# Kernel optimization log

Measured on AMD Instinct MI355X. Metric: run time of the kernel, lower is better.

The kernel has to match this reference:

```python
import jax, jax.numpy as jnp
import numpy as np

B, L, D_MODEL, N_HEADS = 2, 2048, 1024, 16
RANK = max(N_HEADS, int(D_MODEL * 0.25))            # 256
RANK_PER_HEAD = RANK // N_HEADS                      # 16
HEAD_DIM = D_MODEL // N_HEADS                        # 64


def _rope_cos_sin(L, head_dim, dtype=jnp.float32):
    half = head_dim // 2
    theta = 1.0 / (10000.0 ** (jnp.arange(half, dtype=dtype) / half))
    angles = jnp.arange(L, dtype=dtype)[:, None] * theta[None, :]   # [L, half]
    return jnp.cos(angles), jnp.sin(angles)


def _apply_rope(x, cos, sin):
    # x: [B, L, H, D]; pairs (even, odd) rotated by per-position angle.
    B, L, H, D = x.shape
    xp = x.reshape(B, L, H, D // 2, 2)
    x0, x1 = xp[..., 0], xp[..., 1]
    c = cos[None, :, None, :]
    s = sin[None, :, None, :]
    r0 = x0 * c - x1 * s
    r1 = x0 * s + x1 * c
    return jnp.stack([r0, r1], axis=-1).reshape(B, L, H, D)


def setup_inputs() -> dict:
    key = jax.random.key(0)
    ks = jax.random.split(key, 7)
    x = jax.random.normal(ks[0], (B, L, D_MODEL), dtype=jnp.float32)
    mask = jax.random.randint(ks[1], (B, L), 0, 2, dtype=jnp.int32)
    scale = 0.02
    Wq = jax.random.normal(ks[2], (RANK, D_MODEL), dtype=jnp.float32) * scale
    Wk = jax.random.normal(ks[3], (RANK, D_MODEL), dtype=jnp.float32) * scale
    Wv = jax.random.normal(ks[4], (RANK, D_MODEL), dtype=jnp.float32) * scale
    xav_u = float(np.sqrt(6.0 / (HEAD_DIM + RANK_PER_HEAD)))
    U = jax.random.uniform(ks[5], (N_HEADS, HEAD_DIM, RANK_PER_HEAD), dtype=jnp.float32, minval=-xav_u, maxval=xav_u)
    V = jax.random.uniform(ks[6], (N_HEADS, RANK_PER_HEAD, HEAD_DIM), dtype=jnp.float32, minval=-xav_u, maxval=xav_u)
    return {"x": x, "Wq": Wq, "Wk": Wk, "Wv": Wv, "U": U, "V": V, "mask": mask}


def reference(x, Wq, Wk, Wv, U, V, mask):
    Bq, Lq, _ = x.shape
    H, HD, RH = U.shape
    q_low = (x @ Wq.T).reshape(Bq, Lq, H, RH)
    k_low = (x @ Wk.T).reshape(Bq, Lq, H, RH)
    v_low = (x @ Wv.T).reshape(Bq, Lq, H, RH)
    # up-project q/k to head_dim via shared U
    q = jnp.einsum('hdr,blhr->blhd', U, q_low)
    k = jnp.einsum('hdr,blhr->blhd', U, k_low)
    cos, sin = _rope_cos_sin(Lq, HD, x.dtype)
    q = _apply_rope(q, cos, sin)
    k = _apply_rope(k, cos, sin)
    attn = jnp.einsum('blhd,bmhd->bhlm', q, k) / jnp.sqrt(jnp.asarray(HD, x.dtype))
    key_mask = mask.astype(bool)[:, None, None, :]           # [B,1,1,M]
    attn = jnp.where(key_mask, attn, jnp.asarray(-jnp.inf, attn.dtype))
    attn = jax.nn.softmax(attn, axis=-1)
    out = jnp.einsum('bhlm,bmhr->blhr', attn, v_low)
    out = jnp.einsum('blhr,hrd->blhd', out, V)
    return out.reshape(Bq, Lq, H * HD)
```

## Files before the change

kernel.cpp:

```cpp
#include <hip/hip_runtime.h>
#include <hip/hip_bf16.h>

typedef unsigned short u16;
typedef unsigned int u32;
typedef __bf16 bf16x8 __attribute__((ext_vector_type(8)));
typedef float f32x4 __attribute__((ext_vector_type(4)));

#define NB 2
#define NL 2048
#define NDM 1024
#define NH 16
#define NHD 64
#define NRH 16
#define NCOL 2304

#define QSCL 0.18033688011112042f

#define AS1(p) ((const __attribute__((address_space(1))) void*)(p))
#define AS3(p) ((__attribute__((address_space(3))) void*)(p))

__device__ __forceinline__ u16 f2bf(float f) {
  u32 u = __builtin_bit_cast(u32, f);
  u32 r = (u + 0x7fffu + ((u >> 16) & 1u)) >> 16;
  return (u16)r;
}

__global__ void k_prep_weff(const float* __restrict__ Wq, const float* __restrict__ Wk,
                            const float* __restrict__ Wv, const float* __restrict__ U,
                            u16* __restrict__ Wall) {
  int idx = blockIdx.x * 256 + threadIdx.x;
  int col = idx & 1023;
  int row = idx >> 10;
  float acc;
  if (row < 2048) {
    const float* W = (row < 1024) ? Wq : Wk;
    int rr = row & 1023;
    int h = rr >> 6, d = rr & 63;
    const float* Uh = U + (h * NHD + d) * NRH;
    const float* Wr = W + (size_t)(h * NRH) * NDM + col;
    acc = 0.f;
#pragma unroll
    for (int r = 0; r < 16; ++r) acc += Uh[r] * Wr[(size_t)r * NDM];
  } else {
    acc = Wv[(size_t)(row - 2048) * NDM + col];
  }
  Wall[idx] = f2bf(acc);
}

__global__ void k_cast_x(const float* __restrict__ x, u16* __restrict__ xb) {
  int i = blockIdx.x * 256 + threadIdx.x;
  float2 v = *(const float2*)(x + (size_t)i * 2);
  ushort2 o;
  o.x = f2bf(v.x);
  o.y = f2bf(v.y);
  *(ushort2*)(xb + (size_t)i * 2) = o;
}

__global__ void k_cstab(float2* __restrict__ cstab) {
  int i = blockIdx.x * 256 + threadIdx.x;
  if (i >= NL * 32) return;
  int l = i >> 5, j = i & 31;
  float theta = 1.0f / powf(10000.0f, (float)j * (1.0f / 32.0f));
  float ang = (float)l * theta;
  cstab[i] = float2{cosf(ang), sinf(ang)};
}

__global__ void k_fbias(const int* __restrict__ mask, float* __restrict__ fb) {
  int i = blockIdx.x * 256 + threadIdx.x;
  fb[i] = mask[i] ? 0.f : -1e30f;
}

__global__ __launch_bounds__(256) void k_gemm(const u16* __restrict__ A,
                                              const u16* __restrict__ Bm,
                                              const float2* __restrict__ cstab,
                                              u16* __restrict__ qt,
                                              u16* __restrict__ ktb,
                                              u16* __restrict__ vT) {
  __shared__ char lds[32768];
  const int tid = threadIdx.x;
  const int wave = tid >> 6, lane = tid & 63;
  const int bm = blockIdx.x, bn = blockIdx.y;
  const int wr = wave >> 1, wc = wave & 1;
  const char* Ag = (const char*)(A + (size_t)bm * 128 * NDM);
  const char* Bg = (const char*)(Bm + (size_t)bn * 128 * NDM);
  f32x4 acc[4][4] = {};
  for (int kt = 0; kt < 16; ++kt) {
    __syncthreads();
#pragma unroll
    for (int i = 0; i < 4; ++i) {
      int off = wave * 4096 + i * 1024 + lane * 16;
      int src = off ^ ((off >> 3) & 0x70);
      int ga = (src >> 7) * 2048 + kt * 128 + (src & 127);
      __builtin_amdgcn_global_load_lds(AS1(Ag + ga), AS3(lds + wave * 4096 + i * 1024), 16, 0, 0);
      __builtin_amdgcn_global_load_lds(AS1(Bg + ga), AS3(lds + 16384 + wave * 4096 + i * 1024), 16, 0, 0);
    }
    __syncthreads();
#pragma unroll
    for (int kk = 0; kk < 2; ++kk) {
      bf16x8 af[4], bfr[4];
#pragma unroll
      for (int m = 0; m < 4; ++m) {
        int row = wr * 64 + m * 16 + (lane & 15);
        int byte = row * 128 + kk * 64 + ((lane >> 4) << 4);
        af[m] = *(const bf16x8*)(lds + (byte ^ ((row & 7) << 4)));
      }
#pragma unroll
      for (int n = 0; n < 4; ++n) {
        int row = wc * 64 + n * 16 + (lane & 15);
        int byte = row * 128 + kk * 64 + ((lane >> 4) << 4);
        bfr[n] = *(const bf16x8*)(lds + 16384 + (byte ^ ((row & 7) << 4)));
      }
#pragma unroll
      for (int m = 0; m < 4; ++m)
#pragma unroll
        for (int n = 0; n < 4; ++n)
          acc[m][n] = __builtin_amdgcn_mfma_f32_16x16x32_bf16(af[m], bfr[n], acc[m][n], 0, 0, 0);
    }
  }

  const int r0 = bm * 128 + wr * 64;
  const int b = r0 >> 11;
  if (bn < 16) {
    const bool isq = (bn < 8);
    u16* dst = isq ? qt : ktb;
    const float qs = isq ? QSCL : 1.0f;
    const int hh = (isq ? bn : bn - 8) * 2 + wc;
    const int par = lane & 1;
    const size_t base = ((size_t)(b * NH + hh)) * NL;
#pragma unroll
    for (int n = 0; n < 4; ++n) {
      const int d = n * 16 + (lane & 15);
      const int j = d >> 1;
#pragma unroll
      for (int m = 0; m < 4; ++m) {
#pragma unroll
        for (int r = 0; r < 4; ++r) {
          int row = r0 + m * 16 + ((lane >> 4) << 2) + r;
          int l = row & 2047;
          float2 cs = cstab[l * 32 + j];
          float v = acc[m][n][r];
          float pv = __shfl_xor(v, 1);
          float ov = par ? (pv * cs.y + v * cs.x) : (v * cs.x - pv * cs.y);
          dst[((base + l) << 6) + d] = f2bf(ov * qs);
        }
      }
    }
  } else {
    const int rr = lane & 15;
#pragma unroll
    for (int n = 0; n < 4; ++n) {
      const int hh = (bn - 16) * 8 + wc * 4 + n;
      const size_t vbase = ((size_t)(b * NH + hh) * NRH + rr) * NL;
#pragma unroll
      for (int m = 0; m < 4; ++m) {
        int row0 = r0 + m * 16 + ((lane >> 4) << 2);
        int l = row0 & 2047;
        int l6 = l & 63;
        int P = (l & ~63) | (((l6 >> 4) & 1) << 5) | (((l6 >> 5) & 1) << 2) |
                (((l6 >> 2) & 3) << 3) | (l6 & 3);
        ushort4 o4;
        o4.x = f2bf(acc[m][n][0]);
        o4.y = f2bf(acc[m][n][1]);
        o4.z = f2bf(acc[m][n][2]);
        o4.w = f2bf(acc[m][n][3]);
        *(ushort4*)(vT + vbase + P) = o4;
      }
    }
  }
}

__global__ __launch_bounds__(256) void k_attn(const u16* __restrict__ qt,
                                              const u16* __restrict__ ktp,
                                              const u16* __restrict__ vT,
                                              const float* __restrict__ fbias,
                                              float* __restrict__ Oattn) {
  __shared__ char lds[16384];
  const int tid = threadIdx.x, wave = tid >> 6, lane = tid & 63;
  int blk = (int)blockIdx.x;
  blk = (blk & 7) * 128 + (blk >> 3);
  const int qtile = blk & 31, h = (blk >> 5) & 15, b = blk >> 9;
  const size_t bh = (size_t)(b * NH + h);
  const u16* Q = qt + (bh * NL + (size_t)qtile * 64) * 64;
  const u16* K = ktp + bh * NL * 64;
  const u16* Vt = vT + bh * NRH * NL;
  const float* fbb = fbias + b * NL;

  const int g = lane >> 4, qi = lane & 15;
  const int swq = (qi & 7) << 4;

  const int qr = wave * 16 + qi;
  bf16x8 qf0 = *(const bf16x8*)(Q + qr * 64 + g * 8);
  bf16x8 qf1 = *(const bf16x8*)(Q + qr * 64 + 32 + g * 8);

  f32x4 o = {0.f, 0.f, 0.f, 0.f};
  float M = -1e30f, Ls = 0.f;

  const u16* Vrow = Vt + (size_t)qi * NL + g * 8;
  const float* fbg = fbb + g * 4;
  int koff[4][2];
#pragma unroll
  for (int n = 0; n < 4; ++n)
#pragma unroll
    for (int dc = 0; dc < 2; ++dc)
      koff[n][dc] = (((n * 16 + qi) * 128 + dc * 64 + g * 16) ^ swq);

#pragma unroll
  for (int i = 0; i < 2; ++i) {
    int off = wave * 2048 + i * 1024 + lane * 16;
    int src = off ^ ((off >> 3) & 0x70);
    __builtin_amdgcn_global_load_lds(AS1((const char*)K + src),
                                     AS3(lds + wave * 2048 + i * 1024), 16, 0, 0);
  }

  int cur = 0;
  for (int t = 0; t < 32; ++t) {
    __syncthreads();
    if (t < 31) {
      const char* Kg = (const char*)(K + (size_t)(t + 1) * 4096);
      char* Kn = lds + (cur ^ 1) * 8192;
#pragma unroll
      for (int i = 0; i < 2; ++i) {
        int off = wave * 2048 + i * 1024 + lane * 16;
        int src = off ^ ((off >> 3) & 0x70);
        __builtin_amdgcn_global_load_lds(AS1(Kg + src),
                                         AS3(Kn + wave * 2048 + i * 1024), 16, 0, 0);
      }
    }
    const char* Kcur = lds + cur * 8192;

    const float* fbt = fbg + t * 64;
    f32x4 fb0 = *(const f32x4*)(fbt);
    f32x4 fb1 = *(const f32x4*)(fbt + 16);
    f32x4 fb2 = *(const f32x4*)(fbt + 32);
    f32x4 fb3 = *(const f32x4*)(fbt + 48);
    const u16* Vtt = Vrow + t * 64;
    bf16x8 vf0 = *(const bf16x8*)(Vtt);
    bf16x8 vf1 = *(const bf16x8*)(Vtt + 32);

    f32x4 s0, s1, s2, s3;
#define QK(n, dst, fbv)                                                    \
  {                                                                        \
    bf16x8 k0 = *(const bf16x8*)(Kcur + koff[n][0]);                       \
    bf16x8 k1 = *(const bf16x8*)(Kcur + koff[n][1]);                       \
    f32x4 z = __builtin_amdgcn_mfma_f32_16x16x32_bf16(k0, qf0, fbv, 0, 0, 0); \
    dst = __builtin_amdgcn_mfma_f32_16x16x32_bf16(k1, qf1, z, 0, 0, 0);    \
  }
    QK(0, s0, fb0) QK(1, s1, fb1) QK(2, s2, fb2) QK(3, s3, fb3)
#undef QK

    float m0 = fmaxf(fmaxf(s0[0], s0[1]), fmaxf(s0[2], s0[3]));
    float m1 = fmaxf(fmaxf(s1[0], s1[1]), fmaxf(s1[2], s1[3]));
    float m2 = fmaxf(fmaxf(s2[0], s2[1]), fmaxf(s2[2], s2[3]));
    float m3 = fmaxf(fmaxf(s3[0], s3[1]), fmaxf(s3[2], s3[3]));
    float mt = fmaxf(fmaxf(m0, m1), fmaxf(m2, m3));
    mt = fmaxf(mt, __shfl_xor(mt, 16));
    mt = fmaxf(mt, __shfl_xor(mt, 32));

    if (__any(mt > M + 8.f)) {
      float Mn = fmaxf(M, mt);
      float e = __builtin_amdgcn_exp2f(M - Mn);
      M = Mn;
      Ls *= e;
#pragma unroll
      for (int i = 0; i < 4; ++i) o[i] *= __shfl(e, g * 4 + i);
    }

    float p00 = __builtin_amdgcn_exp2f(s0[0] - M), p01 = __builtin_amdgcn_exp2f(s0[1] - M);
    float p02 = __builtin_amdgcn_exp2f(s0[2] - M), p03 = __builtin_amdgcn_exp2f(s0[3] - M);
    float p10 = __builtin_amdgcn_exp2f(s1[0] - M), p11 = __builtin_amdgcn_exp2f(s1[1] - M);
    float p12 = __builtin_amdgcn_exp2f(s1[2] - M), p13 = __builtin_amdgcn_exp2f(s1[3] - M);
    float p20 = __builtin_amdgcn_exp2f(s2[0] - M), p21 = __builtin_amdgcn_exp2f(s2[1] - M);
    float p22 = __builtin_amdgcn_exp2f(s2[2] - M), p23 = __builtin_amdgcn_exp2f(s2[3] - M);
    float p30 = __builtin_amdgcn_exp2f(s3[0] - M), p31 = __builtin_amdgcn_exp2f(s3[1] - M);
    float p32 = __builtin_amdgcn_exp2f(s3[2] - M), p33 = __builtin_amdgcn_exp2f(s3[3] - M);
    float rs = (((p00 + p01) + (p02 + p03)) + ((p10 + p11) + (p12 + p13))) +
               (((p20 + p21) + (p22 + p23)) + ((p30 + p31) + (p32 + p33)));
    rs += __shfl_xor(rs, 16);
    rs += __shfl_xor(rs, 32);
    Ls += rs;

    bf16x8 pf0, pf1;
    pf0[0] = (__bf16)p00; pf0[1] = (__bf16)p01; pf0[2] = (__bf16)p02; pf0[3] = (__bf16)p03;
    pf0[4] = (__bf16)p20; pf0[5] = (__bf16)p21; pf0[6] = (__bf16)p22; pf0[7] = (__bf16)p23;
    pf1[0] = (__bf16)p10; pf1[1] = (__bf16)p11; pf1[2] = (__bf16)p12; pf1[3] = (__bf16)p13;
    pf1[4] = (__bf16)p30; pf1[5] = (__bf16)p31; pf1[6] = (__bf16)p32; pf1[7] = (__bf16)p33;

    o = __builtin_amdgcn_mfma_f32_16x16x32_bf16(pf0, vf0, o, 0, 0, 0);
    o = __builtin_amdgcn_mfma_f32_16x16x32_bf16(pf1, vf1, o, 0, 0, 0);
    cur ^= 1;
  }

  const size_t qrow0 = bh * NL + (size_t)qtile * 64 + wave * 16;
#pragma unroll
  for (int i = 0; i < 4; ++i) {
    float Li = __shfl(Ls, g * 4 + i);
    Oattn[(qrow0 + g * 4 + i) * NRH + qi] = o[i] / Li;
  }
}

__global__ void k_proj(const float* __restrict__ Oattn, const float* __restrict__ V,
                       float* __restrict__ out) {
  int bl = blockIdx.x;
  int b = bl >> 11, l = bl & 2047;
  __shared__ float sO[256];
  int tid = threadIdx.x;
  sO[tid] = Oattn[((size_t)(b * NH + (tid >> 4)) * NL + l) * NRH + (tid & 15)];
  __syncthreads();
#pragma unroll
  for (int p = 0; p < 4; ++p) {
    int h = (tid >> 6) + p * 4;
    int d = tid & 63;
    float acc = 0.f;
    const float* Vh = V + (size_t)(h * NRH) * NHD + d;
    const float* Oh = sO + h * NRH;
#pragma unroll
    for (int r = 0; r < 16; ++r) acc += Oh[r] * Vh[(size_t)r * NHD];
    out[(size_t)bl * NDM + h * NHD + d] = acc;
  }
}

extern "C" void kernel_launch(void* const* d_in, const int* in_sizes, int n_in,
                              void* d_out, int out_size, void* d_ws, size_t ws_size,
                              hipStream_t stream) {
  (void)in_sizes; (void)n_in; (void)out_size; (void)ws_size;
  const float* x  = (const float*)d_in[0];
  const float* Wq = (const float*)d_in[1];
  const float* Wk = (const float*)d_in[2];
  const float* Wv = (const float*)d_in[3];
  const float* U  = (const float*)d_in[4];
  const float* Vm = (const float*)d_in[5];
  const int* mask = (const int*)d_in[6];
  float* out = (float*)d_out;
  char* ws = (char*)d_ws;

  u16* Wall     = (u16*)(ws);
  u16* xb       = (u16*)(ws + 4718592);
  float* Oattn  = (float*)(ws + 13107200);
  float* fbias  = (float*)(ws + 17301504);
  u16* qt       = (u16*)(ws + 31981568);
  u16* ktb      = (u16*)(ws + 40370176);
  u16* vT       = (u16*)(ws + 48758784);
  float2* cstab = (float2*)(ws + 50855936);

  k_prep_weff<<<dim3(9216), dim3(256), 0, stream>>>(Wq, Wk, Wv, U, Wall);
  k_cast_x<<<dim3(8192), dim3(256), 0, stream>>>(x, xb);
  k_cstab<<<dim3(256), dim3(256), 0, stream>>>(cstab);
  k_fbias<<<dim3(16), dim3(256), 0, stream>>>(mask, fbias);
  k_gemm<<<dim3(32, 18), dim3(256), 0, stream>>>(xb, Wall, cstab, qt, ktb, vT);
  k_attn<<<dim3(1024), dim3(256), 0, stream>>>(qt, ktb, vT, fbias, Oattn);
  k_proj<<<dim3(4096), dim3(256), 0, stream>>>(Oattn, Vm, out);
}
```

Before: 132.2 us.

## Split attention over key halves and merge partials in projection kernel

The attention kernel now splits each query tile's key range into two halves, launching twice as many blocks that each process 16 key tiles. Each block writes unnormalized partial outputs plus its running sum and max. The projection kernel then combines the two partials with log-sum-exp rescaling before applying V. The goal is more parallelism and shorter per-block serial loops on a GPU where 1024 blocks may underfill the CUs. The cost is extra partial-result traffic and re-reading Q in both halves.

```diff
diff --git a/kernel.cpp b/kernel.cpp
--- a/kernel.cpp
+++ b/kernel.cpp
@@ -15,6 +15,9 @@
 #define NCOL 2304
 
 #define QSCL 0.18033688011112042f
+
+#define POH 1048576
+#define PLMH 131072
 
 #define AS1(p) ((const __attribute__((address_space(1))) void*)(p))
 #define AS3(p) ((__attribute__((address_space(3))) void*)(p))
@@ -173,17 +176,18 @@
                                               const u16* __restrict__ ktp,
                                               const u16* __restrict__ vT,
                                               const float* __restrict__ fbias,
-                                              float* __restrict__ Oattn) {
+                                              float* __restrict__ Po,
+                                              float* __restrict__ PLM) {
   __shared__ char lds[16384];
   const int tid = threadIdx.x, wave = tid >> 6, lane = tid & 63;
   int blk = (int)blockIdx.x;
-  blk = (blk & 7) * 128 + (blk >> 3);
-  const int qtile = blk & 31, h = (blk >> 5) & 15, b = blk >> 9;
+  blk = (blk & 7) * 256 + (blk >> 3);
+  const int half = blk & 1, qtile = (blk >> 1) & 31, h = (blk >> 6) & 15, b = blk >> 10;
   const size_t bh = (size_t)(b * NH + h);
   const u16* Q = qt + (bh * NL + (size_t)qtile * 64) * 64;
-  const u16* K = ktp + bh * NL * 64;
+  const u16* K = ktp + bh * NL * 64 + (size_t)half * 16 * 4096;
   const u16* Vt = vT + bh * NRH * NL;
-  const float* fbb = fbias + b * NL;
+  const float* fbb = fbias + b * NL + half * 1024;
 
   const int g = lane >> 4, qi = lane & 15;
   const int swq = (qi & 7) << 4;
@@ -195,7 +199,7 @@
   f32x4 o = {0.f, 0.f, 0.f, 0.f};
   float M = -1e30f, Ls = 0.f;
 
-  const u16* Vrow = Vt + (size_t)qi * NL + g * 8;
+  const u16* Vrow = Vt + (size_t)qi * NL + half * 1024 + g * 8;
   const float* fbg = fbb + g * 4;
   int koff[4][2];
 #pragma unroll
@@ -213,9 +217,9 @@
   }
 
   int cur = 0;
-  for (int t = 0; t < 32; ++t) {
+  for (int t = 0; t < 16; ++t) {
     __syncthreads();
-    if (t < 31) {
+    if (t < 15) {
       const char* Kg = (const char*)(K + (size_t)(t + 1) * 4096);
       char* Kn = lds + (cur ^ 1) * 8192;
 #pragma unroll
@@ -290,21 +294,34 @@
     cur ^= 1;
   }
 
+  float* Poh = Po + (size_t)half * POH;
   const size_t qrow0 = bh * NL + (size_t)qtile * 64 + wave * 16;
 #pragma unroll
-  for (int i = 0; i < 4; ++i) {
-    float Li = __shfl(Ls, g * 4 + i);
-    Oattn[(qrow0 + g * 4 + i) * NRH + qi] = o[i] / Li;
-  }
-}
-
-__global__ void k_proj(const float* __restrict__ Oattn, const float* __restrict__ V,
-                       float* __restrict__ out) {
+  for (int i = 0; i < 4; ++i)
+    Poh[(qrow0 + g * 4 + i) * NRH + qi] = o[i];
+  if (g == 0)
+    *(float2*)(PLM + (size_t)half * PLMH + (qrow0 + qi) * 2) = float2{Ls, M};
+}
+
+__global__ void k_proj(const float* __restrict__ Po, const float* __restrict__ PLM,
+                       const float* __restrict__ V, float* __restrict__ out) {
   int bl = blockIdx.x;
   int b = bl >> 11, l = bl & 2047;
   __shared__ float sO[256];
   int tid = threadIdx.x;
-  sO[tid] = Oattn[((size_t)(b * NH + (tid >> 4)) * NL + l) * NRH + (tid & 15)];
+  {
+    int h = tid >> 4, r = tid & 15;
+    size_t idx = (size_t)(b * NH + h) * NL + l;
+    float o1 = Po[idx * NRH + r];
+    float o2 = Po[POH + idx * NRH + r];
+    float2 lm1 = *(const float2*)(PLM + idx * 2);
+    float2 lm2 = *(const float2*)(PLM + PLMH + idx * 2);
+    float M = fmaxf(lm1.y, lm2.y);
+    float e1 = __builtin_amdgcn_exp2f(lm1.y - M);
+    float e2 = __builtin_amdgcn_exp2f(lm2.y - M);
+    float L = lm1.x * e1 + lm2.x * e2;
+    sO[tid] = (o1 * e1 + o2 * e2) / L;
+  }
   __syncthreads();
 #pragma unroll
   for (int p = 0; p < 4; ++p) {
@@ -335,8 +352,9 @@
 
   u16* Wall     = (u16*)(ws);
   u16* xb       = (u16*)(ws + 4718592);
-  float* Oattn  = (float*)(ws + 13107200);
-  float* fbias  = (float*)(ws + 17301504);
+  float* Po     = (float*)(ws + 13107200);
+  float* PLM    = (float*)(ws + 21495808);
+  float* fbias  = (float*)(ws + 22544384);
   u16* qt       = (u16*)(ws + 31981568);
   u16* ktb      = (u16*)(ws + 40370176);
   u16* vT       = (u16*)(ws + 48758784);
@@ -347,6 +365,6 @@
   k_cstab<<<dim3(256), dim3(256), 0, stream>>>(cstab);
   k_fbias<<<dim3(16), dim3(256), 0, stream>>>(mask, fbias);
   k_gemm<<<dim3(32, 18), dim3(256), 0, stream>>>(xb, Wall, cstab, qt, ktb, vT);
-  k_attn<<<dim3(1024), dim3(256), 0, stream>>>(qt, ktb, vT, fbias, Oattn);
-  k_proj<<<dim3(4096), dim3(256), 0, stream>>>(Oattn, Vm, out);
-}
+  k_attn<<<dim3(2048), dim3(256), 0, stream>>>(qt, ktb, vT, fbias, Po, PLM);
+  k_proj<<<dim3(4096), dim3(256), 0, stream>>>(Po, PLM, Vm, out);
+}
```

After: 134.8 us. About the same (+2.0%).
